# Performance work log

Hardware: AMD Instinct MI355X
Metric: run time of the kernel (lower is better)

The kernel has to match this reference:

```python
import math
import jax, jax.numpy as jnp
import numpy as np

B, T, C = 4, 2048, 1024
H = 16
HS = C // H  # head_size = 64

def setup_inputs() -> dict:
    key = jax.random.key(0)
    k1, k2, k3 = jax.random.split(key, 3)
    x = jax.random.normal(k1, (B, T, C), dtype=jnp.float32)
    W_qkv = jax.random.normal(k2, (C, 3 * C), dtype=jnp.float32) * (1.0 / math.sqrt(C))
    W_proj = jax.random.normal(k3, (C, C), dtype=jnp.float32) * (1.0 / math.sqrt(C))
    b_proj = jnp.zeros((C,), dtype=jnp.float32)
    return {"x": x, "W_qkv": W_qkv, "W_proj": W_proj, "b_proj": b_proj}

def reference(x, W_qkv, W_proj, b_proj):
    Bx, Tx, Cx = x.shape
    qkv = x @ W_qkv  # [B,T,3C]
    q, k, v = jnp.split(qkv, 3, axis=-1)
    # [B,T,C] -> [B,H,T,HS]
    def heads(t):
        return t.reshape(Bx, Tx, H, HS).transpose(0, 2, 1, 3)
    q, k, v = heads(q), heads(k), heads(v)
    scores = jnp.einsum('bhqd,bhkd->bhqk', q, k) / math.sqrt(HS)
    causal = jnp.tril(jnp.ones((Tx, Tx), dtype=bool))
    scores = jnp.where(causal, scores, -jnp.inf)
    attn = jax.nn.softmax(scores, axis=-1)
    out = jnp.einsum('bhqk,bhkd->bhqd', attn, v)  # [B,H,T,HS]
    out = out.transpose(0, 2, 1, 3).reshape(Bx, Tx, Cx)
    return out @ W_proj + b_proj
```

## Files before the change

kernel.cpp:

```cpp
#include <hip/hip_runtime.h>
#include <hip/hip_bf16.h>
#include <cstdint>
#include <cstddef>

using bf16 = __hip_bfloat16;
typedef __attribute__((ext_vector_type(8))) short short8;
typedef __attribute__((ext_vector_type(4))) float floatx4;

#define B_ 4
#define T_ 2048
#define C_ 1024
#define H_ 16
#define HS_ 64
#define BT_ (B_*T_)
#define N3C (3*C_)

#define MFMA16(a,b,c) __builtin_amdgcn_mfma_f32_16x16x32_bf16((a),(b),(c),0,0,0)

#if __has_builtin(__builtin_amdgcn_exp2f)
#define EXP2(x) __builtin_amdgcn_exp2f(x)
#else
#define EXP2(x) exp2f(x)
#endif

static __device__ __forceinline__ void gld16(const bf16* g, bf16* l) {
  __builtin_amdgcn_global_load_lds(
      (const __attribute__((address_space(1))) unsigned int*)g,
      (__attribute__((address_space(3))) unsigned int*)l, 16, 0, 0);
}

static __device__ __forceinline__ unsigned short f2bf_us(float x) {
  bf16 b = __float2bfloat16(x);
  return *(unsigned short*)&b;
}

__global__ __launch_bounds__(256)
void k_prep(const float* __restrict__ x, bf16* __restrict__ xb,
            const float* __restrict__ Wqkv, bf16* __restrict__ wqkvT,
            const float* __restrict__ Wproj, bf16* __restrict__ wprojT)
{
  const int bid = blockIdx.x, tid = threadIdx.x;
  __shared__ float tile[64][65];

  if (bid < 4096) {
    const int i = bid*256 + tid;
    const float4 v0 = ((const float4*)x)[2*i];
    const float4 v1 = ((const float4*)x)[2*i + 1];
    union { bf16 b[8]; uint4 u; } cvt;
    cvt.b[0] = __float2bfloat16(v0.x);
    cvt.b[1] = __float2bfloat16(v0.y);
    cvt.b[2] = __float2bfloat16(v0.z);
    cvt.b[3] = __float2bfloat16(v0.w);
    cvt.b[4] = __float2bfloat16(v1.x);
    cvt.b[5] = __float2bfloat16(v1.y);
    cvt.b[6] = __float2bfloat16(v1.z);
    cvt.b[7] = __float2bfloat16(v1.w);
    ((uint4*)xb)[i] = cvt.u;
    return;
  }

  const float* in; bf16* out; int N, n0, k0;
  if (bid < 4864) {
    const int j = bid - 4096;
    in = Wqkv; out = wqkvT; N = N3C;
    n0 = (j % 48) * 64; k0 = (j / 48) * 64;
  } else {
    const int j = bid - 4864;
    in = Wproj; out = wprojT; N = C_;
    n0 = (j % 16) * 64; k0 = (j / 16) * 64;
  }
  const int r = tid >> 6, c = tid & 63;
  #pragma unroll
  for (int j = 0; j < 16; ++j)
    tile[r + j*4][c] = in[(size_t)(k0 + r + j*4) * N + n0 + c];
  __syncthreads();
  #pragma unroll
  for (int j = 0; j < 16; ++j) {
    int rr = r + j*4;
    out[(size_t)(n0 + rr) * C_ + k0 + c] = __float2bfloat16(tile[c][rr]);
  }
}

__global__ __launch_bounds__(512, 1)
void k_gemmqkv(const bf16* __restrict__ A, const bf16* __restrict__ Bt,
               bf16* __restrict__ Qb, bf16* __restrict__ Kb, bf16* __restrict__ Vt)
{
  __shared__ __align__(16) char smem[122880];
  bf16* const sA = (bf16*)smem;
  bf16* const sB = (bf16*)(smem + 49152);

  const int tid  = threadIdx.x;
  const int lane = tid & 63, wave = tid >> 6;
  const int quad = lane >> 4, l16 = lane & 15;
  const int wm = wave >> 2, wn = wave & 3;

  const int g = blockIdx.x;
  const int xcd = g & 7;
  const int local = g >> 3;
  const int nb = local & 7;
  const int mb = (local >> 3) * 8 + xcd;
  const int m0 = mb * 256;
  const int n0q = nb * 128;

  const int ra = tid >> 2;
  const int gc = (tid & 3) ^ ((ra >> 1) & 3);
  const bf16* aptr = A  + (size_t)(m0 + ra) * C_ + gc*8;
  const bf16* bp0  = Bt + (size_t)(n0q + ra) * C_ + gc*8;
  const bf16* bp1  = Bt + (size_t)(1024 + n0q + ra) * C_ + gc*8;
  const bf16* bp2  = Bt + (size_t)(2048 + n0q + ra) * C_ + gc*8;

  floatx4 acc[8][6] = {};
  const int swz = (l16 >> 1) & 3;
  const int aoff = (wm*128 + l16)*32 + (quad ^ swz)*8;
  const int boff = (wn*96  + l16)*32 + (quad ^ swz)*8;

#define STAGE_A(t,s) { bf16* d = sA + (s)*8192;                     \
    gld16(aptr + (t)*32,                  d + tid*8);               \
    gld16(aptr + (size_t)128*C_ + (t)*32, d + 4096 + tid*8); }
#define STAGE_B(t,s) { bf16* d = sB + (s)*12288;                    \
    gld16(bp0 + (t)*32, d + tid*8);                                 \
    gld16(bp1 + (t)*32, d + 4096 + tid*8);                         \
    gld16(bp2 + (t)*32, d + 8192 + tid*8); }

  STAGE_A(0,0); STAGE_B(0,0);
  STAGE_A(1,1); STAGE_B(1,1);

  int cs = 0;
  #pragma unroll 1
  for (int i = 0; i < 32; ++i) {
    const int s2 = (cs >= 1) ? cs - 1 : 2;
    if (i < 31) asm volatile("s_waitcnt vmcnt(5)" ::: "memory");
    else        asm volatile("s_waitcnt vmcnt(0)" ::: "memory");
    __builtin_amdgcn_sched_barrier(0);
    asm volatile("s_barrier" ::: "memory");
    if (i < 30) { STAGE_A(i+2, s2); STAGE_B(i+2, s2); }
    const bf16* sa = sA + cs*8192;
    const bf16* sb = sB + cs*12288;
    short8 bq[6], af[4];
    #pragma unroll
    for (int j = 0; j < 6; ++j)    bq[j]  = *(const short8*)&sb[boff + j*512];
    #pragma unroll
    for (int ii = 0; ii < 4; ++ii) af[ii] = *(const short8*)&sa[aoff + ii*512];
    __builtin_amdgcn_s_setprio(1);
    #pragma unroll
    for (int ii = 0; ii < 4; ++ii)
      #pragma unroll
      for (int j = 0; j < 6; ++j)
        acc[ii][j] = MFMA16(af[ii], bq[j], acc[ii][j]);
    __builtin_amdgcn_s_setprio(0);
    #pragma unroll
    for (int ii = 0; ii < 4; ++ii) af[ii] = *(const short8*)&sa[aoff + (4+ii)*512];
    __builtin_amdgcn_s_setprio(1);
    #pragma unroll
    for (int ii = 0; ii < 4; ++ii)
      #pragma unroll
      for (int j = 0; j < 6; ++j)
        acc[4+ii][j] = MFMA16(af[ii], bq[j], acc[4+ii][j]);
    __builtin_amdgcn_s_setprio(0);
    cs = (cs == 2) ? 0 : cs + 1;
  }
#undef STAGE_A
#undef STAGE_B

  #pragma unroll
  for (int ii = 0; ii < 8; ++ii) {
    const int rowb = m0 + wm*128 + ii*16 + quad*4;
    #pragma unroll
    for (int j = 0; j < 6; ++j) {
      const int L = wn*96 + j*16 + l16;
      if (L < 256) {
        const int gcol = (L < 128) ? (n0q + L) : (1024 + n0q + L - 128);
        const int h = (gcol >> 6) & 15, d = gcol & 63;
        #pragma unroll
        for (int r = 0; r < 4; ++r) {
          const int rr = rowb + r;
          const int b = rr >> 11, t = rr & 2047;
          const size_t addr = (((size_t)(b*H_ + h) * T_ + t) << 6) + d;
          if (L < 128) Qb[addr] = __float2bfloat16(acc[ii][j][r] * 0.18033688f);
          else         Kb[addr] = __float2bfloat16(acc[ii][j][r]);
        }
      }
    }
  }

  __syncthreads();
  unsigned short* epi = (unsigned short*)smem;
  #pragma unroll
  for (int ii = 0; ii < 8; ++ii) {
    const int tl = wm*128 + ii*16 + quad*4;
    #pragma unroll
    for (int j = 0; j < 6; ++j) {
      const int L = wn*96 + j*16 + l16;
      if (L >= 256) {
        const int ccl = L - 256;
        #pragma unroll
        for (int r = 0; r < 4; ++r)
          epi[ccl*258 + tl + r] = f2bf_us(acc[ii][j][r]);
      }
    }
  }
  __syncthreads();
  const int b  = m0 >> 11;
  const int t0 = m0 & 2047;
  #pragma unroll
  for (int it = 0; it < 32; ++it) {
    const int id = it*512 + tid;
    const int tp = id & 31;
    const int rest = id >> 5;
    const int tl64 = (rest & 3) * 64;
    const int ccl = rest >> 2;
    const int k0p = tp + (tp & 16);
    const unsigned lo = epi[ccl*258 + tl64 + k0p];
    const unsigned hi = epi[ccl*258 + tl64 + k0p + 16];
    const int h = nb*2 + (ccl >> 6), d = ccl & 63;
    unsigned* row = (unsigned*)(Vt + ((size_t)(b*H_ + h) * HS_ + d) * T_);
    row[(t0 >> 1) + tl64/2 + tp] = lo | (hi << 16);
  }
}

template<int NB>
__global__ __launch_bounds__(256, 2)
void k_proj(const bf16* __restrict__ A, const bf16* __restrict__ Bt,
            int N, int K, float* __restrict__ Out, const float* __restrict__ bias)
{
  __shared__ __align__(16) char smem[65536];
  bf16* const sA = (bf16*)smem;
  bf16* const sB = (bf16*)(smem + 32768);

  const int tid  = threadIdx.x;
  const int lane = tid & 63, wave = tid >> 6;
  const int quad = lane >> 4, l16 = lane & 15;
  const int wm = wave >> 1, wn = wave & 1;

  const int g = blockIdx.x;
  const int xcd = g & 7;
  const int local = g >> 3;
  const int nb = local % NB;
  const int mb = (local / NB) * 8 + xcd;
  const int m0 = mb * 128, n0 = nb * 128;

  const int ra = tid >> 2;
  const int gc = (tid & 3) ^ ((ra >> 1) & 3);
  const bf16* aptr = A  + (size_t)(m0 + ra) * K + gc*8;
  const bf16* bptr = Bt + (size_t)(n0 + ra) * K + gc*8;
  const size_t rj = (size_t)64 * K;

  const int KT = K >> 5;
  floatx4 acc[4][4] = {};
  const int swz = (l16 >> 1) & 3;
  const int aoff = (wm*64 + l16)*32 + (quad ^ swz)*8;
  const int boff = (wn*64 + l16)*32 + (quad ^ swz)*8;

  #pragma unroll
  for (int t = 0; t < 3; ++t) {
    bf16* sa = sA + t*4096; bf16* sb = sB + t*4096;
    gld16(aptr + t*32,      sa + tid*8);
    gld16(aptr + rj + t*32, sa + 2048 + tid*8);
    gld16(bptr + t*32,      sb + tid*8);
    gld16(bptr + rj + t*32, sb + 2048 + tid*8);
  }

  #pragma unroll 1
  for (int i = 0; i < KT; ++i) {
    if (i < KT-2)       asm volatile("s_waitcnt vmcnt(8)" ::: "memory");
    else if (i == KT-2) asm volatile("s_waitcnt vmcnt(4)" ::: "memory");
    else                asm volatile("s_waitcnt vmcnt(0)" ::: "memory");
    asm volatile("s_barrier" ::: "memory");
    if (i < KT-3) {
      const int t = i + 3;
      bf16* sa = sA + (t & 3)*4096; bf16* sb = sB + (t & 3)*4096;
      gld16(aptr + t*32,      sa + tid*8);
      gld16(aptr + rj + t*32, sa + 2048 + tid*8);
      gld16(bptr + t*32,      sb + tid*8);
      gld16(bptr + rj + t*32, sb + 2048 + tid*8);
    }
    const bf16* sa = sA + (i & 3)*4096;
    const bf16* sb = sB + (i & 3)*4096;
    short8 af[4], bfm[4];
    #pragma unroll
    for (int ii = 0; ii < 4; ++ii) af[ii]  = *(const short8*)&sa[aoff + ii*512];
    #pragma unroll
    for (int j = 0; j < 4; ++j)    bfm[j]  = *(const short8*)&sb[boff + j*512];
    __builtin_amdgcn_s_setprio(1);
    #pragma unroll
    for (int ii = 0; ii < 4; ++ii)
      #pragma unroll
      for (int j = 0; j < 4; ++j)
        acc[ii][j] = MFMA16(af[ii], bfm[j], acc[ii][j]);
    __builtin_amdgcn_s_setprio(0);
  }

  #pragma unroll
  for (int i = 0; i < 4; ++i) {
    const int rowb = m0 + wm*64 + i*16 + quad*4;
    #pragma unroll
    for (int j = 0; j < 4; ++j) {
      const int col = n0 + wn*64 + j*16 + l16;
      #pragma unroll
      for (int r = 0; r < 4; ++r)
        Out[(size_t)(rowb + r) * N + col] = acc[i][j][r] + bias[col];
    }
  }
}

__global__ __launch_bounds__(256, 3)
void k_attn(const bf16* __restrict__ Q, const bf16* __restrict__ K,
            const bf16* __restrict__ Vt, bf16* __restrict__ att)
{
  __shared__ bf16 kbuf[2][64*64];
  __shared__ bf16 vbuf[2][64*64];
  __shared__ bf16 pbuf[4][32*64];

  const int tid  = threadIdx.x;
  const int lane = tid & 63, wave = tid >> 6;
  const int quad = lane >> 4, l16 = lane & 15;
  const int x7 = l16 & 7;

  const int g  = blockIdx.x;
  const int bh = (g & 7) * 8 + ((g >> 3) & 7);
  const int qt = 15 - (g >> 6);
  const int b = bh >> 4, h = bh & 15;

  const bf16* Qp = Q  + (size_t)bh * T_ * HS_;
  const bf16* Kp = K  + (size_t)bh * T_ * HS_;
  const bf16* Vp = Vt + (size_t)bh * HS_ * T_;

  const int qbase = qt*128 + wave*32;
  const int ntk = 2*qt + 2;

  short8 qf[2][2];
  #pragma unroll
  for (int mt = 0; mt < 2; ++mt)
    #pragma unroll
    for (int ss = 0; ss < 2; ++ss)
      qf[mt][ss] = *(const short8*)(Qp + (size_t)(qbase + mt*16 + l16) * HS_ + ss*32 + quad*8);

  floatx4 o[2][4] = {};
  float lrow[2][4] = {};

  const bf16* kg[2]; const bf16* vg[2];
  int ldsoff[2];
  #pragma unroll
  for (int it = 0; it < 2; ++it) {
    const int c = it*256 + tid;
    const int row = c >> 3;
    const int col = (c & 7) ^ (row & 7);
    kg[it] = Kp + (size_t)row * HS_ + col*8;
    vg[it] = Vp + (size_t)row * T_ + col*8;
    ldsoff[it] = c*8;
  }

  bf16* pw = pbuf[wave];
  unsigned int* pw32 = (unsigned int*)pw;
  const int c0 = l16 >> 2;
  const int dwl = l16 & 3;

  for (int i = 0; i <= ntk; ++i) {
    __syncthreads();
    if (i < ntk) {
      const int stk0 = i * 64;
      bf16* kb = kbuf[i & 1];
      bf16* vb = vbuf[i & 1];
      #pragma unroll
      for (int it = 0; it < 2; ++it) {
        gld16(kg[it] + (size_t)stk0 * HS_, kb + ldsoff[it]);
        gld16(vg[it] + stk0,               vb + ldsoff[it]);
      }
    }
    if (i == 0) continue;
    const int tk  = i - 1;
    const int tk0 = tk * 64;
    if (tk0 > qbase + 31) continue;
    const bf16* kb = kbuf[tk & 1];
    const bf16* vb = vbuf[tk & 1];

    floatx4 s[2][4] = {};
    __builtin_amdgcn_s_setprio(1);
    #pragma unroll
    for (int nt = 0; nt < 4; ++nt) {
      const int key = nt*16 + l16;
      #pragma unroll
      for (int ss = 0; ss < 2; ++ss) {
        short8 kf = *(const short8*)&kb[(key*8 + ((ss*4+quad) ^ x7))*8];
        s[0][nt] = MFMA16(qf[0][ss], kf, s[0][nt]);
        s[1][nt] = MFMA16(qf[1][ss], kf, s[1][nt]);
      }
    }
    __builtin_amdgcn_s_setprio(0);

    if (tk0 + 63 > qbase) {
      #pragma unroll
      for (int mt = 0; mt < 2; ++mt)
        #pragma unroll
        for (int nt = 0; nt < 4; ++nt) {
          const int key = tk0 + nt*16 + l16;
          #pragma unroll
          for (int r = 0; r < 4; ++r) {
            const int qr = qbase + mt*16 + quad*4 + r;
            if (key > qr) s[mt][nt][r] = -1e30f;
          }
        }
    }

    #pragma unroll
    for (int mt = 0; mt < 2; ++mt) {
      #pragma unroll
      for (int r = 0; r < 4; ++r) {
        const float p0 = EXP2(s[mt][0][r]), p1 = EXP2(s[mt][1][r]);
        const float p2 = EXP2(s[mt][2][r]), p3 = EXP2(s[mt][3][r]);
        lrow[mt][r] += (p0 + p1) + (p2 + p3);
        const int q = mt*16 + quad*4 + r;
        const unsigned w0 = __builtin_amdgcn_perm(__float_as_uint(p1), __float_as_uint(p0), 0x07060302u);
        const unsigned w1 = __builtin_amdgcn_perm(__float_as_uint(p3), __float_as_uint(p2), 0x07060302u);
        pw32[q*32 + (((c0 + q)     & 7) << 2) + dwl] = w0;
        pw32[q*32 + (((c0 + q + 4) & 7) << 2) + dwl] = w1;
      }
    }

    __builtin_amdgcn_s_setprio(1);
    #pragma unroll
    for (int ss = 0; ss < 2; ++ss) {
      short8 pf0 = *(const short8*)&pw[l16*64      + ((4*ss + quad + l16) & 7)*8];
      short8 pf1 = *(const short8*)&pw[(16+l16)*64 + ((4*ss + quad + l16) & 7)*8];
      #pragma unroll
      for (int nd = 0; nd < 4; ++nd) {
        const int d = nd*16 + l16;
        short8 vf = *(const short8*)&vb[(d*8 + ((ss*4+quad) ^ x7))*8];
        o[0][nd] = MFMA16(pf0, vf, o[0][nd]);
        o[1][nd] = MFMA16(pf1, vf, o[1][nd]);
      }
    }
    __builtin_amdgcn_s_setprio(0);
  }

  #pragma unroll
  for (int mt = 0; mt < 2; ++mt) {
    #pragma unroll
    for (int r = 0; r < 4; ++r) {
      float lsum = lrow[mt][r];
      lsum += __shfl_xor(lsum, 1);
      lsum += __shfl_xor(lsum, 2);
      lsum += __shfl_xor(lsum, 4);
      lsum += __shfl_xor(lsum, 8);
      const float inv = 1.0f / lsum;
      const int tt = qbase + mt*16 + quad*4 + r;
      #pragma unroll
      for (int nd = 0; nd < 4; ++nd)
        att[(size_t)(b*T_ + tt) * C_ + h*64 + nd*16 + l16] =
            __float2bfloat16(o[mt][nd][r] * inv);
    }
  }
}

extern "C" void kernel_launch(void* const* d_in, const int* in_sizes, int n_in,
                              void* d_out, int out_size, void* d_ws, size_t ws_size,
                              hipStream_t stream) {
  const float* x     = (const float*)d_in[0];
  const float* Wqkv  = (const float*)d_in[1];
  const float* Wproj = (const float*)d_in[2];
  const float* bproj = (const float*)d_in[3];
  float* out = (float*)d_out;

  char* ws = (char*)d_ws;
  bf16* xb     = (bf16*)(ws + 0);
  bf16* wqkvT  = (bf16*)(ws + 16777216);
  bf16* wprojT = (bf16*)(ws + 23068672);
  bf16* Qb     = (bf16*)(ws + 25165824);
  bf16* Kb     = (bf16*)(ws + 41943040);
  bf16* Vt     = (bf16*)(ws + 58720256);
  bf16* att    = (bf16*)(ws + 75497472);

  k_prep<<<dim3(5120), 256, 0, stream>>>(x, xb, Wqkv, wqkvT, Wproj, wprojT);
  k_gemmqkv<<<dim3(256), 512, 0, stream>>>(xb, wqkvT, Qb, Kb, Vt);
  k_attn<<<dim3(1024), 256, 0, stream>>>(Qb, Kb, Vt, att);
  k_proj<8><<<dim3(512), 256, 0, stream>>>(
      att, wprojT, C_, C_, out, bproj);
}
```

Measured before the change: 216.7 us.

## Load K and V fragments directly from global memory, dropping LDS staging

```diff
diff --git a/kernel.cpp b/kernel.cpp
--- a/kernel.cpp
+++ b/kernel.cpp
@@ -307,14 +307,11 @@
 void k_attn(const bf16* __restrict__ Q, const bf16* __restrict__ K,
             const bf16* __restrict__ Vt, bf16* __restrict__ att)
 {
-  __shared__ bf16 kbuf[2][64*64];
-  __shared__ bf16 vbuf[2][64*64];
   __shared__ bf16 pbuf[4][32*64];
 
   const int tid  = threadIdx.x;
   const int lane = tid & 63, wave = tid >> 6;
   const int quad = lane >> 4, l16 = lane & 15;
-  const int x7 = l16 & 7;
 
   const int g  = blockIdx.x;
   const int bh = (g & 7) * 8 + ((g >> 3) & 7);
@@ -338,50 +335,27 @@
   floatx4 o[2][4] = {};
   float lrow[2][4] = {};
 
-  const bf16* kg[2]; const bf16* vg[2];
-  int ldsoff[2];
-  #pragma unroll
-  for (int it = 0; it < 2; ++it) {
-    const int c = it*256 + tid;
-    const int row = c >> 3;
-    const int col = (c & 7) ^ (row & 7);
-    kg[it] = Kp + (size_t)row * HS_ + col*8;
-    vg[it] = Vp + (size_t)row * T_ + col*8;
-    ldsoff[it] = c*8;
-  }
+  const bf16* kbase = Kp + (size_t)l16 * HS_ + quad*8;
+  const bf16* vbase = Vp + (size_t)l16 * T_  + quad*8;
 
   bf16* pw = pbuf[wave];
   unsigned int* pw32 = (unsigned int*)pw;
   const int c0 = l16 >> 2;
   const int dwl = l16 & 3;
 
-  for (int i = 0; i <= ntk; ++i) {
-    __syncthreads();
-    if (i < ntk) {
-      const int stk0 = i * 64;
-      bf16* kb = kbuf[i & 1];
-      bf16* vb = vbuf[i & 1];
-      #pragma unroll
-      for (int it = 0; it < 2; ++it) {
-        gld16(kg[it] + (size_t)stk0 * HS_, kb + ldsoff[it]);
-        gld16(vg[it] + stk0,               vb + ldsoff[it]);
-      }
-    }
-    if (i == 0) continue;
-    const int tk  = i - 1;
+  #pragma unroll 1
+  for (int tk = 0; tk < ntk; ++tk) {
     const int tk0 = tk * 64;
-    if (tk0 > qbase + 31) continue;
-    const bf16* kb = kbuf[tk & 1];
-    const bf16* vb = vbuf[tk & 1];
+    if (tk0 > qbase + 31) break;
 
     floatx4 s[2][4] = {};
     __builtin_amdgcn_s_setprio(1);
     #pragma unroll
     for (int nt = 0; nt < 4; ++nt) {
-      const int key = nt*16 + l16;
+      const bf16* kr = kbase + (size_t)(tk0 + nt*16) * HS_;
       #pragma unroll
       for (int ss = 0; ss < 2; ++ss) {
-        short8 kf = *(const short8*)&kb[(key*8 + ((ss*4+quad) ^ x7))*8];
+        short8 kf = *(const short8*)(kr + ss*32);
         s[0][nt] = MFMA16(qf[0][ss], kf, s[0][nt]);
         s[1][nt] = MFMA16(qf[1][ss], kf, s[1][nt]);
       }
@@ -424,8 +398,7 @@
       short8 pf1 = *(const short8*)&pw[(16+l16)*64 + ((4*ss + quad + l16) & 7)*8];
       #pragma unroll
       for (int nd = 0; nd < 4; ++nd) {
-        const int d = nd*16 + l16;
-        short8 vf = *(const short8*)&vb[(d*8 + ((ss*4+quad) ^ x7))*8];
+        short8 vf = *(const short8*)(vbase + (size_t)(nd*16) * T_ + tk0 + ss*32);
         o[0][nd] = MFMA16(pf0, vf, o[0][nd]);
         o[1][nd] = MFMA16(pf1, vf, o[1][nd]);
       }
```

Result: slower. 303.0 us (+39.8%).
